# Optimization experiments

Measured on AMD Instinct MI355X. Metric: run time of the kernel, lower is better.

The kernel has to match this reference:

```python
import jax, jax.numpy as jnp
import numpy as np


def setup_inputs() -> dict:
    key = jax.random.key(0)
    ks = jax.random.split(key, 16)
    B, S, H = 512, 128, 256
    f32 = jnp.float32
    inputs = jax.random.normal(ks[0], (B, S, 2), f32)
    # xavier-normal-ish init (gain/sqrt(fan_in+fan_out) approximated by small scale)
    def xn(k, shape):
        fan = shape[0] + shape[1]
        return jax.random.normal(k, shape, f32) * np.sqrt(2.0 / fan)
    return {
        "inputs": inputs,
        "W0": xn(ks[1], (H, 2)),   "b0": jnp.zeros((H,), f32),
        "W1": xn(ks[2], (H, H)),   "b1": jnp.zeros((H,), f32),
        "W2": xn(ks[3], (H, H)),   "b2": jnp.zeros((H,), f32),
        "W3": xn(ks[4], (H, H)),   "b3": jnp.zeros((H,), f32),
        "W4": xn(ks[5], (1, H)),   "b4": jnp.zeros((1,), f32),
        "log_growth_rate": jax.random.normal(ks[6], (), f32),
        "log_carrying_capacity": jax.random.normal(ks[7], (), f32),
        "log_initial_loss": jax.random.normal(ks[8], (), f32),
        "in_mean": jnp.array([0.5, 50.0], f32),
        "in_std": jnp.array([0.2, 30.0], f32),
        "tgt_mean": jnp.array([0.8], f32),
        "tgt_std": jnp.array([0.1], f32),
    }


def reference(inputs, W0, b0, W1, b1, W2, b2, W3, b3, W4, b4,
              log_growth_rate, log_carrying_capacity, log_initial_loss,
              in_mean, in_std, tgt_mean, tgt_std):
    B, S = inputs.shape[0], inputs.shape[1]
    # PDE parameters (Verhulst logistic growth)
    r = jnp.exp(-log_growth_rate)
    K = 0.2 + (1.0 - 0.2) * jax.nn.sigmoid(log_carrying_capacity)  # carrying capacity in [0.2, 1]
    C = 0.0 + (0.1 - 0.0) * jax.nn.sigmoid(log_initial_loss)       # initial loss in [0, 0.1]

    # split state feature s and time t, standardize per-column
    s = inputs[..., 0:1].reshape(-1, 1)  # [N,1]
    t = inputs[..., 1:2].reshape(-1, 1)  # [N,1]
    s_norm = (s - in_mean[0:1]) / (in_std[0:1] + 1e-8)
    t_norm = (t - in_mean[1:2]) / (in_std[1:2] + 1e-8)

    Ws = (W0, W1, W2, W3, W4)
    bs = (b0, b1, b2, b3, b4)

    def mlp(x):  # [N,2] -> [N,1], tanh MLP
        h = x
        for W, b in zip(Ws[:-1], bs[:-1]):
            h = jnp.tanh(h @ W.T + b)
        return h @ Ws[-1].T + bs[-1]

    def u_of(tn):  # U(s_norm, tn), inverse-standardized targets
        return mlp(jnp.concatenate([s_norm, tn], axis=-1)) * tgt_std + tgt_mean

    ones = jnp.ones_like(t_norm)

    def uf_of(tn):
        # U and U_t = dU/dt_norm (forward-mode; each point depends on its own scalar t)
        U, U_dot = jax.jvp(u_of, (tn,), (ones,))
        U_t = U_dot.sum(-1, keepdims=True)
        G = r * (U - C) * (1.0 - (U - C) / (K - C))  # Verhulst
        return U, U_t - G  # (U, F)

    # second derivative w.r.t. t_norm: F_t = U_tt - G_t
    (U, F), (_, F_t) = jax.jvp(uf_of, (t_norm,), (ones,))

    shp = (B, S, 1)
    return U.reshape(shp), F.reshape(shp), F_t.reshape(shp)
```

## Files before the change

kernel.cpp:

```cpp
#include <hip/hip_runtime.h>
#include <hip/hip_bf16.h>
#include <math.h>

typedef short s8v __attribute__((ext_vector_type(8)));
typedef float f4v __attribute__((ext_vector_type(4)));

#define HH 256
#define TP 16
#define NTHREADS 256
#define KSTR 520
#define TSTR 4160
#define NTILES 3
#define PLANE (NTILES * TSTR)

__device__ __forceinline__ unsigned short bf_rne(float x){
    union{float f;unsigned u;}v; v.f=x;
    unsigned r = v.u + 0x7FFFu + ((v.u >> 16) & 1u);
    return (unsigned short)(r >> 16);
}
__device__ __forceinline__ unsigned pack_rne2(float a, float b){
    union { __hip_bfloat162 h; unsigned u; } v;
    v.h = __float22bfloat162_rn(float2{a, b});
    return v.u;
}

__global__ __launch_bounds__(256)
void prep_weights(const float* __restrict__ W1, const float* __restrict__ W2,
                  const float* __restrict__ W3, const float* __restrict__ W0,
                  const float* __restrict__ b0, const float* __restrict__ W4,
                  unsigned short* __restrict__ wsB, float* __restrict__ wsF)
{
    int t = blockIdx.x * 256 + threadIdx.x;
    if (t < 24576) {
        int layer = t >> 13;
        int rem = t & 8191;
        int l  = rem & 63;
        int ks = (rem >> 6) & 7;
        int nt = rem >> 9;
        const float* W = (layer == 0) ? W1 : (layer == 1) ? W2 : W3;
        int n_out = nt * 16 + (l & 15);
        int quad  = l >> 4;
        const float* row = W + n_out * HH;
        s8v hi;
        #pragma unroll
        for (int j = 0; j < 8; ++j) {
            int n_in = quad * 64 + (j & 3) * 16 + ((j >> 2) << 3) + ks;
            hi[j] = (short)bf_rne(row[n_in]);
        }
        int dst = ((nt * 8 + ks) * 64 + l) * 8;
        *(s8v*)(wsB + layer * 65536 + dst) = hi;
    } else if (t < 24832) {
        int n = t - 24576;
        int pos = ((n & 7) * 4 + (n >> 6)) * 8 + ((n >> 4) & 3) + 4 * ((n >> 3) & 1);
        wsF[pos]       = W0[2 * n];
        wsF[256 + pos] = W0[2 * n + 1];
        wsF[512 + pos] = b0[n];
        wsF[768 + pos] = W4[n];
    }
}

__global__ __launch_bounds__(NTHREADS, 4)
void capnn_mfma(const float* __restrict__ inp,
                const float* __restrict__ b1, const float* __restrict__ b2,
                const float* __restrict__ b3, const float* __restrict__ b4,
                const float* __restrict__ W4raw,
                const float* __restrict__ lgr, const float* __restrict__ lcc,
                const float* __restrict__ lil,
                const float* __restrict__ imean, const float* __restrict__ istd,
                const float* __restrict__ tmean, const float* __restrict__ tstd,
                const unsigned short* __restrict__ wsW,
                const float* __restrict__ wsF,
                float* __restrict__ out, int N)
{
    __shared__ __align__(16) unsigned short Ahi[PLANE];
    __shared__ float sn_sh[TP], tn_sh[TP];
    __shared__ float head_part[TP * 3 * 4];

    const int tid  = threadIdx.x;
    const int lane = tid & 63;
    const int w    = tid >> 6;
    const int m16  = lane & 15;
    const int q    = lane >> 4;
    const int pbase = blockIdx.x * TP;

    const float* __restrict__ w00p = wsF;
    const float* __restrict__ w01p = wsF + 256;
    const float* __restrict__ b0p  = wsF + 512;

    if (tid < TP) {
        int pg = pbase + tid;
        float s = 0.f, t = 0.f;
        if (pg < N) { s = inp[2 * pg]; t = inp[2 * pg + 1]; }
        sn_sh[tid] = (s - imean[0]) / (istd[0] + 1e-8f);
        tn_sh[tid] = (t - imean[1]) / (istd[1] + 1e-8f);
    }
    __syncthreads();

    {
        const int l  = lane;
        const int p16 = l & 15, quad = l >> 4;
        const float sn = sn_sh[p16], tn = tn_sh[p16];
        #pragma unroll
        for (int g2 = 0; g2 < 2; ++g2) {
            const int ks = w + 4 * g2;
            const int pos = (ks * 4 + quad) * 8;
            float4 wA0 = *(const float4*)(w00p + pos);
            float4 wA1 = *(const float4*)(w00p + pos + 4);
            float4 wB0 = *(const float4*)(w01p + pos);
            float4 wB1 = *(const float4*)(w01p + pos + 4);
            float4 bb0 = *(const float4*)(b0p + pos);
            float4 bb1 = *(const float4*)(b0p + pos + 4);
            float w00v[8] = {wA0.x,wA0.y,wA0.z,wA0.w,wA1.x,wA1.y,wA1.z,wA1.w};
            float w01v[8] = {wB0.x,wB0.y,wB0.z,wB0.w,wB1.x,wB1.y,wB1.z,wB1.w};
            float b0v[8]  = {bb0.x,bb0.y,bb0.z,bb0.w,bb1.x,bb1.y,bb1.z,bb1.w};
            const int base = ks * KSTR + l * 8;
            float av[8], d1v[8], d2v[8];
            #pragma unroll
            for (int j = 0; j < 8; ++j) {
                float z = fmaf(w00v[j], sn, fmaf(w01v[j], tn, b0v[j]));
                float e = __expf(2.f * z);
                float a = 1.f - 2.f * __builtin_amdgcn_rcpf(e + 1.f);
                float g = 1.f - a * a;
                float d1 = g * w01v[j];
                float d2 = -2.f * a * d1 * w01v[j];
                av[j] = a; d1v[j] = d1; d2v[j] = d2;
            }
            #pragma unroll
            for (int s = 0; s < 3; ++s) {
                const float* V = (s == 0) ? av : (s == 1) ? d1v : d2v;
                int4 hi4;
                hi4.x = (int)pack_rne2(V[0], V[1]);
                hi4.y = (int)pack_rne2(V[2], V[3]);
                hi4.z = (int)pack_rne2(V[4], V[5]);
                hi4.w = (int)pack_rne2(V[6], V[7]);
                *(int4*)&Ahi[s * TSTR + base] = hi4;
            }
        }
    }
    __syncthreads();

    for (int L = 0; L < 3; ++L) {
        const unsigned short* __restrict__ Wlh = wsW + L * 65536;
        const float* __restrict__ bL = (L == 0) ? b1 : (L == 1) ? b2 : b3;

        f4v acc[NTILES][4];
        #pragma unroll
        for (int i = 0; i < 4; ++i) {
            float bias = bL[w * 64 + i * 16 + m16];
            acc[0][i] = (f4v){bias, bias, bias, bias};
            acc[1][i] = (f4v){0.f, 0.f, 0.f, 0.f};
            acc[2][i] = (f4v){0.f, 0.f, 0.f, 0.f};
        }

        __builtin_amdgcn_s_setprio(1);
        #pragma unroll
        for (int ks = 0; ks < 8; ++ks) {
            s8v ah[NTILES];
            const int aoff = ks * KSTR + lane * 8;
            #pragma unroll
            for (int t = 0; t < NTILES; ++t)
                ah[t] = *(const s8v*)&Ahi[t * TSTR + aoff];
            #pragma unroll
            for (int i = 0; i < 4; ++i) {
                const int off = (((w * 4 + i) * 8 + ks) * 64 + lane) * 8;
                s8v bh = *(const s8v*)(Wlh + off);
                #pragma unroll
                for (int t = 0; t < NTILES; ++t)
                    acc[t][i] = __builtin_amdgcn_mfma_f32_16x16x32_bf16(ah[t], bh, acc[t][i], 0, 0, 0);
            }
        }
        __builtin_amdgcn_s_setprio(0);

        if (L < 2) {
            __syncthreads();
            const int ksw  = m16 & 7;
            const int hsel = m16 >> 3;
            const int wbase = ksw * KSTR + (16 * w + q * 4) * 8 + 4 * hsel;
            #pragma unroll
            for (int r = 0; r < 4; ++r) {
                float Av[3][4];
                #pragma unroll
                for (int i = 0; i < 4; ++i) {
                    float z  = acc[0][i][r];
                    float z1 = acc[1][i][r];
                    float z2 = acc[2][i][r];
                    float e = __expf(2.f * z);
                    float a = 1.f - 2.f * __builtin_amdgcn_rcpf(e + 1.f);
                    float g = 1.f - a * a;
                    float d1 = g * z1;
                    float d2 = fmaf(g, z2, -2.f * a * d1 * z1);
                    Av[0][i] = a; Av[1][i] = d1; Av[2][i] = d2;
                }
                #pragma unroll
                for (int s = 0; s < 3; ++s) {
                    int2 hi2;
                    hi2.x = (int)pack_rne2(Av[s][0], Av[s][1]);
                    hi2.y = (int)pack_rne2(Av[s][2], Av[s][3]);
                    *(int2*)&Ahi[s * TSTR + wbase + r * 8] = hi2;
                }
            }
            __syncthreads();
        } else {
            float w4v[4];
            #pragma unroll
            for (int i = 0; i < 4; ++i) w4v[i] = W4raw[w * 64 + i * 16 + m16];

            float hp[3][4];
            #pragma unroll
            for (int s = 0; s < 3; ++s)
                #pragma unroll
                for (int r = 0; r < 4; ++r) hp[s][r] = 0.f;
            #pragma unroll
            for (int r = 0; r < 4; ++r) {
                #pragma unroll
                for (int i = 0; i < 4; ++i) {
                    float z  = acc[0][i][r];
                    float z1 = acc[1][i][r];
                    float z2 = acc[2][i][r];
                    float e = __expf(2.f * z);
                    float a = 1.f - 2.f * __builtin_amdgcn_rcpf(e + 1.f);
                    float g = 1.f - a * a;
                    float d1 = g * z1;
                    float d2 = fmaf(g, z2, -2.f * a * d1 * z1);
                    hp[0][r] = fmaf(w4v[i], a,  hp[0][r]);
                    hp[1][r] = fmaf(w4v[i], d1, hp[1][r]);
                    hp[2][r] = fmaf(w4v[i], d2, hp[2][r]);
                }
            }
            #pragma unroll
            for (int m = 1; m < 16; m <<= 1) {
                #pragma unroll
                for (int s = 0; s < 3; ++s)
                    #pragma unroll
                    for (int r = 0; r < 4; ++r)
                        hp[s][r] += __shfl_xor(hp[s][r], m);
            }
            if (m16 == 0) {
                #pragma unroll
                for (int s = 0; s < 3; ++s)
                    #pragma unroll
                    for (int r = 0; r < 4; ++r)
                        head_part[(s * TP + q * 4 + r) * 4 + w] = hp[s][r];
            }
            __syncthreads();
        }
    }

    if (tid < TP) {
        float sv = 0.f, s1v = 0.f, s2v = 0.f;
        #pragma unroll
        for (int ww = 0; ww < 4; ++ww) {
            sv  += head_part[(0 * TP + tid) * 4 + ww];
            s1v += head_part[(1 * TP + tid) * 4 + ww];
            s2v += head_part[(2 * TP + tid) * 4 + ww];
        }
        int pg = pbase + tid;
        if (pg < N) {
            float r_  = expf(-lgr[0]);
            float Kc  = 0.2f + 0.8f / (1.f + expf(-lcc[0]));
            float Cc  = 0.1f / (1.f + expf(-lil[0]));
            float kci = 1.f / (Kc - Cc);
            float ts = tstd[0], tm = tmean[0];
            float U   = (sv + b4[0]) * ts + tm;
            float Ut  = s1v * ts;
            float Utt = s2v * ts;
            float Um  = U - Cc;
            float G   = r_ * Um * (1.f - Um * kci);
            float Gt  = r_ * Ut * (1.f - 2.f * Um * kci);
            out[pg]         = U;
            out[N + pg]     = Ut - G;
            out[2 * N + pg] = Utt - Gt;
        }
    }
}

extern "C" void kernel_launch(void* const* d_in, const int* in_sizes, int n_in,
                              void* d_out, int out_size, void* d_ws, size_t ws_size,
                              hipStream_t stream) {
    const float* inp   = (const float*)d_in[0];
    const float* W0    = (const float*)d_in[1];
    const float* b0    = (const float*)d_in[2];
    const float* W1    = (const float*)d_in[3];
    const float* b1    = (const float*)d_in[4];
    const float* W2    = (const float*)d_in[5];
    const float* b2    = (const float*)d_in[6];
    const float* W3    = (const float*)d_in[7];
    const float* b3    = (const float*)d_in[8];
    const float* W4    = (const float*)d_in[9];
    const float* b4    = (const float*)d_in[10];
    const float* lgr   = (const float*)d_in[11];
    const float* lcc   = (const float*)d_in[12];
    const float* lil   = (const float*)d_in[13];
    const float* imean = (const float*)d_in[14];
    const float* istd  = (const float*)d_in[15];
    const float* tmean = (const float*)d_in[16];
    const float* tstd  = (const float*)d_in[17];

    unsigned short* wsB = (unsigned short*)d_ws;
    float* wsF = (float*)((char*)d_ws + 393216);

    const int N = in_sizes[0] / 2;
    const int gridMain = (N + TP - 1) / TP;

    hipLaunchKernelGGL(prep_weights, dim3(97), dim3(256), 0, stream,
                       W1, W2, W3, W0, b0, W4, wsB, wsF);
    hipLaunchKernelGGL(capnn_mfma, dim3(gridMain), dim3(NTHREADS), 0, stream,
                       inp, b1, b2, b3, b4, W4,
                       lgr, lcc, lil, imean, istd, tmean, tstd,
                       wsB, wsF, (float*)d_out, N);
}
```

Before: 180.4 us.

## Process three 16-point groups per block to reuse weight fragments across more MFMA tiles

Each block now handles 48 points instead of 16, so 9 MFMA accumulator tiles share each loaded weight fragment instead of 3. This cuts global weight loads per point threefold. In exchange it roughly triples LDS use and accumulator registers, and launch bounds drop from 4 to 2 blocks per CU, which lowers occupancy.

```diff
diff --git a/kernel.cpp b/kernel.cpp
--- a/kernel.cpp
+++ b/kernel.cpp
@@ -6,11 +6,12 @@
 typedef float f4v __attribute__((ext_vector_type(4)));
 
 #define HH 256
-#define TP 16
+#define TP 48
 #define NTHREADS 256
+#define NGRP 3
 #define KSTR 520
 #define TSTR 4160
-#define NTILES 3
+#define NTILES 9
 #define PLANE (NTILES * TSTR)
 
 __device__ __forceinline__ unsigned short bf_rne(float x){
@@ -59,7 +60,7 @@
     }
 }
 
-__global__ __launch_bounds__(NTHREADS, 4)
+__global__ __launch_bounds__(NTHREADS, 2)
 void capnn_mfma(const float* __restrict__ inp,
                 const float* __restrict__ b1, const float* __restrict__ b2,
                 const float* __restrict__ b3, const float* __restrict__ b4,
@@ -99,7 +100,6 @@
     {
         const int l  = lane;
         const int p16 = l & 15, quad = l >> 4;
-        const float sn = sn_sh[p16], tn = tn_sh[p16];
         #pragma unroll
         for (int g2 = 0; g2 < 2; ++g2) {
             const int ks = w + 4 * g2;
@@ -114,26 +114,30 @@
             float w01v[8] = {wB0.x,wB0.y,wB0.z,wB0.w,wB1.x,wB1.y,wB1.z,wB1.w};
             float b0v[8]  = {bb0.x,bb0.y,bb0.z,bb0.w,bb1.x,bb1.y,bb1.z,bb1.w};
             const int base = ks * KSTR + l * 8;
-            float av[8], d1v[8], d2v[8];
-            #pragma unroll
-            for (int j = 0; j < 8; ++j) {
-                float z = fmaf(w00v[j], sn, fmaf(w01v[j], tn, b0v[j]));
-                float e = __expf(2.f * z);
-                float a = 1.f - 2.f * __builtin_amdgcn_rcpf(e + 1.f);
-                float g = 1.f - a * a;
-                float d1 = g * w01v[j];
-                float d2 = -2.f * a * d1 * w01v[j];
-                av[j] = a; d1v[j] = d1; d2v[j] = d2;
-            }
-            #pragma unroll
-            for (int s = 0; s < 3; ++s) {
-                const float* V = (s == 0) ? av : (s == 1) ? d1v : d2v;
-                int4 hi4;
-                hi4.x = (int)pack_rne2(V[0], V[1]);
-                hi4.y = (int)pack_rne2(V[2], V[3]);
-                hi4.z = (int)pack_rne2(V[4], V[5]);
-                hi4.w = (int)pack_rne2(V[6], V[7]);
-                *(int4*)&Ahi[s * TSTR + base] = hi4;
+            #pragma unroll
+            for (int h = 0; h < NGRP; ++h) {
+                const float sn = sn_sh[h * 16 + p16], tn = tn_sh[h * 16 + p16];
+                float av[8], d1v[8], d2v[8];
+                #pragma unroll
+                for (int j = 0; j < 8; ++j) {
+                    float z = fmaf(w00v[j], sn, fmaf(w01v[j], tn, b0v[j]));
+                    float e = __expf(2.f * z);
+                    float a = 1.f - 2.f * __builtin_amdgcn_rcpf(e + 1.f);
+                    float g = 1.f - a * a;
+                    float d1 = g * w01v[j];
+                    float d2 = -2.f * a * d1 * w01v[j];
+                    av[j] = a; d1v[j] = d1; d2v[j] = d2;
+                }
+                #pragma unroll
+                for (int s = 0; s < 3; ++s) {
+                    const float* V = (s == 0) ? av : (s == 1) ? d1v : d2v;
+                    int4 hi4;
+                    hi4.x = (int)pack_rne2(V[0], V[1]);
+                    hi4.y = (int)pack_rne2(V[2], V[3]);
+                    hi4.z = (int)pack_rne2(V[4], V[5]);
+                    hi4.w = (int)pack_rne2(V[6], V[7]);
+                    *(int4*)&Ahi[(s * NGRP + h) * TSTR + base] = hi4;
+                }
             }
         }
     }
@@ -147,9 +151,10 @@
         #pragma unroll
         for (int i = 0; i < 4; ++i) {
             float bias = bL[w * 64 + i * 16 + m16];
-            acc[0][i] = (f4v){bias, bias, bias, bias};
-            acc[1][i] = (f4v){0.f, 0.f, 0.f, 0.f};
-            acc[2][i] = (f4v){0.f, 0.f, 0.f, 0.f};
+            #pragma unroll
+            for (int t = 0; t < NTILES; ++t)
+                acc[t][i] = (t < NGRP) ? (f4v){bias, bias, bias, bias}
+                                       : (f4v){0.f, 0.f, 0.f, 0.f};
         }
 
         __builtin_amdgcn_s_setprio(1);
@@ -177,26 +182,29 @@
             const int hsel = m16 >> 3;
             const int wbase = ksw * KSTR + (16 * w + q * 4) * 8 + 4 * hsel;
             #pragma unroll
-            for (int r = 0; r < 4; ++r) {
-                float Av[3][4];
-                #pragma unroll
-                for (int i = 0; i < 4; ++i) {
-                    float z  = acc[0][i][r];
-                    float z1 = acc[1][i][r];
-                    float z2 = acc[2][i][r];
-                    float e = __expf(2.f * z);
-                    float a = 1.f - 2.f * __builtin_amdgcn_rcpf(e + 1.f);
-                    float g = 1.f - a * a;
-                    float d1 = g * z1;
-                    float d2 = fmaf(g, z2, -2.f * a * d1 * z1);
-                    Av[0][i] = a; Av[1][i] = d1; Av[2][i] = d2;
-                }
-                #pragma unroll
-                for (int s = 0; s < 3; ++s) {
-                    int2 hi2;
-                    hi2.x = (int)pack_rne2(Av[s][0], Av[s][1]);
-                    hi2.y = (int)pack_rne2(Av[s][2], Av[s][3]);
-                    *(int2*)&Ahi[s * TSTR + wbase + r * 8] = hi2;
+            for (int h = 0; h < NGRP; ++h) {
+                #pragma unroll
+                for (int r = 0; r < 4; ++r) {
+                    float Av[3][4];
+                    #pragma unroll
+                    for (int i = 0; i < 4; ++i) {
+                        float z  = acc[0 * NGRP + h][i][r];
+                        float z1 = acc[1 * NGRP + h][i][r];
+                        float z2 = acc[2 * NGRP + h][i][r];
+                        float e = __expf(2.f * z);
+                        float a = 1.f - 2.f * __builtin_amdgcn_rcpf(e + 1.f);
+                        float g = 1.f - a * a;
+                        float d1 = g * z1;
+                        float d2 = fmaf(g, z2, -2.f * a * d1 * z1);
+                        Av[0][i] = a; Av[1][i] = d1; Av[2][i] = d2;
+                    }
+                    #pragma unroll
+                    for (int s = 0; s < 3; ++s) {
+                        int2 hi2;
+                        hi2.x = (int)pack_rne2(Av[s][0], Av[s][1]);
+                        hi2.y = (int)pack_rne2(Av[s][2], Av[s][3]);
+                        *(int2*)&Ahi[(s * NGRP + h) * TSTR + wbase + r * 8] = hi2;
+                    }
                 }
             }
             __syncthreads();
@@ -205,42 +213,45 @@
             #pragma unroll
             for (int i = 0; i < 4; ++i) w4v[i] = W4raw[w * 64 + i * 16 + m16];
 
-            float hp[3][4];
-            #pragma unroll
-            for (int s = 0; s < 3; ++s)
-                #pragma unroll
-                for (int r = 0; r < 4; ++r) hp[s][r] = 0.f;
-            #pragma unroll
-            for (int r = 0; r < 4; ++r) {
-                #pragma unroll
-                for (int i = 0; i < 4; ++i) {
-                    float z  = acc[0][i][r];
-                    float z1 = acc[1][i][r];
-                    float z2 = acc[2][i][r];
-                    float e = __expf(2.f * z);
-                    float a = 1.f - 2.f * __builtin_amdgcn_rcpf(e + 1.f);
-                    float g = 1.f - a * a;
-                    float d1 = g * z1;
-                    float d2 = fmaf(g, z2, -2.f * a * d1 * z1);
-                    hp[0][r] = fmaf(w4v[i], a,  hp[0][r]);
-                    hp[1][r] = fmaf(w4v[i], d1, hp[1][r]);
-                    hp[2][r] = fmaf(w4v[i], d2, hp[2][r]);
-                }
-            }
-            #pragma unroll
-            for (int m = 1; m < 16; m <<= 1) {
+            #pragma unroll
+            for (int h = 0; h < NGRP; ++h) {
+                float hp[3][4];
                 #pragma unroll
                 for (int s = 0; s < 3; ++s)
                     #pragma unroll
-                    for (int r = 0; r < 4; ++r)
-                        hp[s][r] += __shfl_xor(hp[s][r], m);
-            }
-            if (m16 == 0) {
-                #pragma unroll
-                for (int s = 0; s < 3; ++s)
-                    #pragma unroll
-                    for (int r = 0; r < 4; ++r)
-                        head_part[(s * TP + q * 4 + r) * 4 + w] = hp[s][r];
+                    for (int r = 0; r < 4; ++r) hp[s][r] = 0.f;
+                #pragma unroll
+                for (int r = 0; r < 4; ++r) {
+                    #pragma unroll
+                    for (int i = 0; i < 4; ++i) {
+                        float z  = acc[0 * NGRP + h][i][r];
+                        float z1 = acc[1 * NGRP + h][i][r];
+                        float z2 = acc[2 * NGRP + h][i][r];
+                        float e = __expf(2.f * z);
+                        float a = 1.f - 2.f * __builtin_amdgcn_rcpf(e + 1.f);
+                        float g = 1.f - a * a;
+                        float d1 = g * z1;
+                        float d2 = fmaf(g, z2, -2.f * a * d1 * z1);
+                        hp[0][r] = fmaf(w4v[i], a,  hp[0][r]);
+                        hp[1][r] = fmaf(w4v[i], d1, hp[1][r]);
+                        hp[2][r] = fmaf(w4v[i], d2, hp[2][r]);
+                    }
+                }
+                #pragma unroll
+                for (int m = 1; m < 16; m <<= 1) {
+                    #pragma unroll
+                    for (int s = 0; s < 3; ++s)
+                        #pragma unroll
+                        for (int r = 0; r < 4; ++r)
+                            hp[s][r] += __shfl_xor(hp[s][r], m);
+                }
+                if (m16 == 0) {
+                    #pragma unroll
+                    for (int s = 0; s < 3; ++s)
+                        #pragma unroll
+                        for (int r = 0; r < 4; ++r)
+                            head_part[(s * TP + h * 16 + q * 4 + r) * 4 + w] = hp[s][r];
+                }
             }
             __syncthreads();
         }
```

After: 187.5 us. +4.0%, slower.

## Switch to 32x32x16 MFMA tiles with 32 points per block

Applied to the files above, without the earlier changes.

Replaces the 16x16x32 bf16 MFMA scheme with 32x32x16 MFMAs, doubles points per block to 32, and re-lays out packed weights and LDS activations to match. Each wave now computes two 32-column tiles for the three tangent planes, and the tanh/derivative transform writes scalar bf16 values back to shared memory. The aim is more work per weight fetch and higher MFMA throughput. In exchange it needs more registers (occupancy hint drops from 4 to 3 blocks per CU), makes LDS stores scalar, and drops the padded strides, which may cause bank conflicts.

```diff
diff --git a/kernel.cpp b/kernel.cpp
--- a/kernel.cpp
+++ b/kernel.cpp
@@ -2,16 +2,13 @@
 #include <hip/hip_bf16.h>
 #include <math.h>
 
-typedef short s8v __attribute__((ext_vector_type(8)));
-typedef float f4v __attribute__((ext_vector_type(4)));
+typedef short s8v  __attribute__((ext_vector_type(8)));
+typedef float f16v __attribute__((ext_vector_type(16)));
 
 #define HH 256
-#define TP 16
+#define TP 32
 #define NTHREADS 256
-#define KSTR 520
-#define TSTR 4160
-#define NTILES 3
-#define PLANE (NTILES * TSTR)
+#define SSTR 8192
 
 __device__ __forceinline__ unsigned short bf_rne(float x){
     union{float f;unsigned u;}v; v.f=x;
@@ -33,33 +30,124 @@
     int t = blockIdx.x * 256 + threadIdx.x;
     if (t < 24576) {
         int layer = t >> 13;
-        int rem = t & 8191;
-        int l  = rem & 63;
-        int ks = (rem >> 6) & 7;
-        int nt = rem >> 9;
+        int rem   = t & 8191;
+        int lane  = rem & 63;
+        int kstep = (rem >> 6) & 15;
+        int ct    = rem >> 10;
         const float* W = (layer == 0) ? W1 : (layer == 1) ? W2 : W3;
-        int n_out = nt * 16 + (l & 15);
-        int quad  = l >> 4;
-        const float* row = W + n_out * HH;
+        int row  = ct * 32 + (lane & 31);
+        int nin0 = kstep * 16 + (lane >> 5) * 8;
+        const float* src = W + row * HH + nin0;
         s8v hi;
         #pragma unroll
-        for (int j = 0; j < 8; ++j) {
-            int n_in = quad * 64 + (j & 3) * 16 + ((j >> 2) << 3) + ks;
-            hi[j] = (short)bf_rne(row[n_in]);
-        }
-        int dst = ((nt * 8 + ks) * 64 + l) * 8;
-        *(s8v*)(wsB + layer * 65536 + dst) = hi;
+        for (int j = 0; j < 8; ++j) hi[j] = (short)bf_rne(src[j]);
+        int dst = layer * 65536 + ct * 8192 + kstep * 512 + lane * 8;
+        *(s8v*)(wsB + dst) = hi;
     } else if (t < 24832) {
         int n = t - 24576;
-        int pos = ((n & 7) * 4 + (n >> 6)) * 8 + ((n >> 4) & 3) + 4 * ((n >> 3) & 1);
-        wsF[pos]       = W0[2 * n];
-        wsF[256 + pos] = W0[2 * n + 1];
-        wsF[512 + pos] = b0[n];
-        wsF[768 + pos] = W4[n];
-    }
-}
-
-__global__ __launch_bounds__(NTHREADS, 4)
+        wsF[n]       = W0[2 * n];
+        wsF[256 + n] = W0[2 * n + 1];
+        wsF[512 + n] = b0[n];
+        wsF[768 + n] = W4[n];
+    }
+}
+
+__device__ __forceinline__ void mfma_layer32(
+    f16v (&acc)[3][2], const unsigned short* Ahi,
+    const unsigned short* __restrict__ Wlh,
+    float biasA, float biasB, int lane)
+{
+    #pragma unroll
+    for (int r = 0; r < 16; ++r) {
+        acc[0][0][r] = biasA; acc[0][1][r] = biasB;
+        acc[1][0][r] = 0.f;   acc[1][1][r] = 0.f;
+        acc[2][0][r] = 0.f;   acc[2][1][r] = 0.f;
+    }
+    __builtin_amdgcn_s_setprio(1);
+    #pragma unroll
+    for (int k = 0; k < 16; ++k) {
+        const int ab = k * 512 + lane * 8;
+        s8v a0 = *(const s8v*)&Ahi[ab];
+        s8v a1 = *(const s8v*)&Ahi[SSTR + ab];
+        s8v a2 = *(const s8v*)&Ahi[2 * SSTR + ab];
+        s8v b0 = *(const s8v*)&Wlh[ab];
+        s8v b1 = *(const s8v*)&Wlh[8192 + ab];
+        acc[0][0] = __builtin_amdgcn_mfma_f32_32x32x16_bf16(a0, b0, acc[0][0], 0, 0, 0);
+        acc[1][0] = __builtin_amdgcn_mfma_f32_32x32x16_bf16(a1, b0, acc[1][0], 0, 0, 0);
+        acc[2][0] = __builtin_amdgcn_mfma_f32_32x32x16_bf16(a2, b0, acc[2][0], 0, 0, 0);
+        acc[0][1] = __builtin_amdgcn_mfma_f32_32x32x16_bf16(a0, b1, acc[0][1], 0, 0, 0);
+        acc[1][1] = __builtin_amdgcn_mfma_f32_32x32x16_bf16(a1, b1, acc[1][1], 0, 0, 0);
+        acc[2][1] = __builtin_amdgcn_mfma_f32_32x32x16_bf16(a2, b1, acc[2][1], 0, 0, 0);
+    }
+    __builtin_amdgcn_s_setprio(0);
+}
+
+__device__ __forceinline__ void transform32(
+    f16v (&acc)[3][2], unsigned short* Ahi, int w, int lane)
+{
+    const int col = lane & 31, half = lane >> 5;
+    #pragma unroll
+    for (int cti = 0; cti < 2; ++cti) {
+        const int kst   = (2 * w + cti) * 2 + (col >> 4);
+        const int basec = kst * 512 + ((col >> 3) & 1) * 256 + (col & 7);
+        #pragma unroll
+        for (int reg = 0; reg < 16; ++reg) {
+            const int rP = (reg & 3) + 8 * (reg >> 2) + 4 * half;
+            float z  = acc[0][cti][reg];
+            float z1 = acc[1][cti][reg];
+            float z2 = acc[2][cti][reg];
+            float e  = __expf(2.f * z);
+            float a  = 1.f - 2.f * __builtin_amdgcn_rcpf(e + 1.f);
+            float g  = 1.f - a * a;
+            float d1 = g * z1;
+            float d2 = fmaf(g, z2, -2.f * a * d1 * z1);
+            const int sa = basec + rP * 8;
+            Ahi[sa]            = bf_rne(a);
+            Ahi[SSTR + sa]     = bf_rne(d1);
+            Ahi[2 * SSTR + sa] = bf_rne(d2);
+        }
+    }
+}
+
+__device__ __forceinline__ void head32(
+    f16v (&acc)[3][2], const float* __restrict__ wsF,
+    float* head_part, int w, int lane)
+{
+    const int col = lane & 31, half = lane >> 5;
+    const float w4a = wsF[768 + (2 * w) * 32 + col];
+    const float w4b = wsF[768 + (2 * w + 1) * 32 + col];
+    #pragma unroll
+    for (int reg = 0; reg < 16; ++reg) {
+        float ha = 0.f, h1 = 0.f, h2 = 0.f;
+        #pragma unroll
+        for (int cti = 0; cti < 2; ++cti) {
+            float z  = acc[0][cti][reg];
+            float z1 = acc[1][cti][reg];
+            float z2 = acc[2][cti][reg];
+            float e  = __expf(2.f * z);
+            float a  = 1.f - 2.f * __builtin_amdgcn_rcpf(e + 1.f);
+            float g  = 1.f - a * a;
+            float d1 = g * z1;
+            float d2 = fmaf(g, z2, -2.f * a * d1 * z1);
+            float w4 = cti ? w4b : w4a;
+            ha = fmaf(w4, a, ha); h1 = fmaf(w4, d1, h1); h2 = fmaf(w4, d2, h2);
+        }
+        #pragma unroll
+        for (int m = 1; m < 32; m <<= 1) {
+            ha += __shfl_xor(ha, m);
+            h1 += __shfl_xor(h1, m);
+            h2 += __shfl_xor(h2, m);
+        }
+        if (col == 0) {
+            const int rP = (reg & 3) + 8 * (reg >> 2) + 4 * half;
+            head_part[(0 * TP + rP) * 4 + w] = ha;
+            head_part[(1 * TP + rP) * 4 + w] = h1;
+            head_part[(2 * TP + rP) * 4 + w] = h2;
+        }
+    }
+}
+
+__global__ __launch_bounds__(NTHREADS, 3)
 void capnn_mfma(const float* __restrict__ inp,
                 const float* __restrict__ b1, const float* __restrict__ b2,
                 const float* __restrict__ b3, const float* __restrict__ b4,
@@ -72,20 +160,15 @@
                 const float* __restrict__ wsF,
                 float* __restrict__ out, int N)
 {
-    __shared__ __align__(16) unsigned short Ahi[PLANE];
+    __shared__ __align__(16) unsigned short Ahi[3 * SSTR];
     __shared__ float sn_sh[TP], tn_sh[TP];
     __shared__ float head_part[TP * 3 * 4];
 
     const int tid  = threadIdx.x;
     const int lane = tid & 63;
     const int w    = tid >> 6;
-    const int m16  = lane & 15;
-    const int q    = lane >> 4;
+    const int col  = lane & 31;
     const int pbase = blockIdx.x * TP;
-
-    const float* __restrict__ w00p = wsF;
-    const float* __restrict__ w01p = wsF + 256;
-    const float* __restrict__ b0p  = wsF + 512;
 
     if (tid < TP) {
         int pg = pbase + tid;
@@ -97,34 +180,33 @@
     __syncthreads();
 
     {
-        const int l  = lane;
-        const int p16 = l & 15, quad = l >> 4;
-        const float sn = sn_sh[p16], tn = tn_sh[p16];
-        #pragma unroll
-        for (int g2 = 0; g2 < 2; ++g2) {
-            const int ks = w + 4 * g2;
-            const int pos = (ks * 4 + quad) * 8;
-            float4 wA0 = *(const float4*)(w00p + pos);
-            float4 wA1 = *(const float4*)(w00p + pos + 4);
-            float4 wB0 = *(const float4*)(w01p + pos);
-            float4 wB1 = *(const float4*)(w01p + pos + 4);
-            float4 bb0 = *(const float4*)(b0p + pos);
-            float4 bb1 = *(const float4*)(b0p + pos + 4);
-            float w00v[8] = {wA0.x,wA0.y,wA0.z,wA0.w,wA1.x,wA1.y,wA1.z,wA1.w};
-            float w01v[8] = {wB0.x,wB0.y,wB0.z,wB0.w,wB1.x,wB1.y,wB1.z,wB1.w};
+        const int p = lane & 31, c = lane >> 5;
+        const float sn = sn_sh[p], tn = tn_sh[p];
+        #pragma unroll
+        for (int g = 0; g < 4; ++g) {
+            const int m  = w + 4 * g;
+            const int nb = m * 16 + c * 8;
+            float4 wa0 = *(const float4*)(wsF + nb);
+            float4 wa1 = *(const float4*)(wsF + nb + 4);
+            float4 wb0 = *(const float4*)(wsF + 256 + nb);
+            float4 wb1 = *(const float4*)(wsF + 256 + nb + 4);
+            float4 bb0 = *(const float4*)(wsF + 512 + nb);
+            float4 bb1 = *(const float4*)(wsF + 512 + nb + 4);
+            float w00v[8] = {wa0.x,wa0.y,wa0.z,wa0.w,wa1.x,wa1.y,wa1.z,wa1.w};
+            float w01v[8] = {wb0.x,wb0.y,wb0.z,wb0.w,wb1.x,wb1.y,wb1.z,wb1.w};
             float b0v[8]  = {bb0.x,bb0.y,bb0.z,bb0.w,bb1.x,bb1.y,bb1.z,bb1.w};
-            const int base = ks * KSTR + l * 8;
             float av[8], d1v[8], d2v[8];
             #pragma unroll
             for (int j = 0; j < 8; ++j) {
                 float z = fmaf(w00v[j], sn, fmaf(w01v[j], tn, b0v[j]));
                 float e = __expf(2.f * z);
                 float a = 1.f - 2.f * __builtin_amdgcn_rcpf(e + 1.f);
-                float g = 1.f - a * a;
-                float d1 = g * w01v[j];
+                float g2 = 1.f - a * a;
+                float d1 = g2 * w01v[j];
                 float d2 = -2.f * a * d1 * w01v[j];
                 av[j] = a; d1v[j] = d1; d2v[j] = d2;
             }
+            const int base = m * 512 + lane * 8;
             #pragma unroll
             for (int s = 0; s < 3; ++s) {
                 const float* V = (s == 0) ? av : (s == 1) ? d1v : d2v;
@@ -133,118 +215,30 @@
                 hi4.y = (int)pack_rne2(V[2], V[3]);
                 hi4.z = (int)pack_rne2(V[4], V[5]);
                 hi4.w = (int)pack_rne2(V[6], V[7]);
-                *(int4*)&Ahi[s * TSTR + base] = hi4;
+                *(int4*)&Ahi[s * SSTR + base] = hi4;
             }
         }
     }
     __syncthreads();
 
-    for (int L = 0; L < 3; ++L) {
-        const unsigned short* __restrict__ Wlh = wsW + L * 65536;
-        const float* __restrict__ bL = (L == 0) ? b1 : (L == 1) ? b2 : b3;
-
-        f4v acc[NTILES][4];
-        #pragma unroll
-        for (int i = 0; i < 4; ++i) {
-            float bias = bL[w * 64 + i * 16 + m16];
-            acc[0][i] = (f4v){bias, bias, bias, bias};
-            acc[1][i] = (f4v){0.f, 0.f, 0.f, 0.f};
-            acc[2][i] = (f4v){0.f, 0.f, 0.f, 0.f};
-        }
-
-        __builtin_amdgcn_s_setprio(1);
-        #pragma unroll
-        for (int ks = 0; ks < 8; ++ks) {
-            s8v ah[NTILES];
-            const int aoff = ks * KSTR + lane * 8;
-            #pragma unroll
-            for (int t = 0; t < NTILES; ++t)
-                ah[t] = *(const s8v*)&Ahi[t * TSTR + aoff];
-            #pragma unroll
-            for (int i = 0; i < 4; ++i) {
-                const int off = (((w * 4 + i) * 8 + ks) * 64 + lane) * 8;
-                s8v bh = *(const s8v*)(Wlh + off);
-                #pragma unroll
-                for (int t = 0; t < NTILES; ++t)
-                    acc[t][i] = __builtin_amdgcn_mfma_f32_16x16x32_bf16(ah[t], bh, acc[t][i], 0, 0, 0);
-            }
-        }
-        __builtin_amdgcn_s_setprio(0);
-
-        if (L < 2) {
-            __syncthreads();
-            const int ksw  = m16 & 7;
-            const int hsel = m16 >> 3;
-            const int wbase = ksw * KSTR + (16 * w + q * 4) * 8 + 4 * hsel;
-            #pragma unroll
-            for (int r = 0; r < 4; ++r) {
-                float Av[3][4];
-                #pragma unroll
-                for (int i = 0; i < 4; ++i) {
-                    float z  = acc[0][i][r];
-                    float z1 = acc[1][i][r];
-                    float z2 = acc[2][i][r];
-                    float e = __expf(2.f * z);
-                    float a = 1.f - 2.f * __builtin_amdgcn_rcpf(e + 1.f);
-                    float g = 1.f - a * a;
-                    float d1 = g * z1;
-                    float d2 = fmaf(g, z2, -2.f * a * d1 * z1);
-                    Av[0][i] = a; Av[1][i] = d1; Av[2][i] = d2;
-                }
-                #pragma unroll
-                for (int s = 0; s < 3; ++s) {
-                    int2 hi2;
-                    hi2.x = (int)pack_rne2(Av[s][0], Av[s][1]);
-                    hi2.y = (int)pack_rne2(Av[s][2], Av[s][3]);
-                    *(int2*)&Ahi[s * TSTR + wbase + r * 8] = hi2;
-                }
-            }
-            __syncthreads();
-        } else {
-            float w4v[4];
-            #pragma unroll
-            for (int i = 0; i < 4; ++i) w4v[i] = W4raw[w * 64 + i * 16 + m16];
-
-            float hp[3][4];
-            #pragma unroll
-            for (int s = 0; s < 3; ++s)
-                #pragma unroll
-                for (int r = 0; r < 4; ++r) hp[s][r] = 0.f;
-            #pragma unroll
-            for (int r = 0; r < 4; ++r) {
-                #pragma unroll
-                for (int i = 0; i < 4; ++i) {
-                    float z  = acc[0][i][r];
-                    float z1 = acc[1][i][r];
-                    float z2 = acc[2][i][r];
-                    float e = __expf(2.f * z);
-                    float a = 1.f - 2.f * __builtin_amdgcn_rcpf(e + 1.f);
-                    float g = 1.f - a * a;
-                    float d1 = g * z1;
-                    float d2 = fmaf(g, z2, -2.f * a * d1 * z1);
-                    hp[0][r] = fmaf(w4v[i], a,  hp[0][r]);
-                    hp[1][r] = fmaf(w4v[i], d1, hp[1][r]);
-                    hp[2][r] = fmaf(w4v[i], d2, hp[2][r]);
-                }
-            }
-            #pragma unroll
-            for (int m = 1; m < 16; m <<= 1) {
-                #pragma unroll
-                for (int s = 0; s < 3; ++s)
-                    #pragma unroll
-                    for (int r = 0; r < 4; ++r)
-                        hp[s][r] += __shfl_xor(hp[s][r], m);
-            }
-            if (m16 == 0) {
-                #pragma unroll
-                for (int s = 0; s < 3; ++s)
-                    #pragma unroll
-                    for (int r = 0; r < 4; ++r)
-                        head_part[(s * TP + q * 4 + r) * 4 + w] = hp[s][r];
-            }
-            __syncthreads();
-        }
-    }
+    f16v acc[3][2];
+
+    mfma_layer32(acc, Ahi, wsW + (2 * w) * 8192,
+                 b1[(2 * w) * 32 + col], b1[(2 * w + 1) * 32 + col], lane);
+    __syncthreads();
+    transform32(acc, Ahi, w, lane);
+    __syncthreads();
+
+    mfma_layer32(acc, Ahi, wsW + 65536 + (2 * w) * 8192,
+                 b2[(2 * w) * 32 + col], b2[(2 * w + 1) * 32 + col], lane);
+    __syncthreads();
+    transform32(acc, Ahi, w, lane);
+    __syncthreads();
+
+    mfma_layer32(acc, Ahi, wsW + 131072 + (2 * w) * 8192,
+                 b3[(2 * w) * 32 + col], b3[(2 * w + 1) * 32 + col], lane);
+    head32(acc, wsF, head_part, w, lane);
+    __syncthreads();
 
     if (tid < TP) {
         float sv = 0.f, s1v = 0.f, s2v = 0.f;
```

Result: slower. 202.8 us (+12.4%).
